# Optimization experiments

Measured on AMD Instinct MI355X. Metric: run time of the kernel, lower is better.

Reference implementation:

```python
import jax, jax.numpy as jnp
import numpy as np

D_MODEL = 1024
H = 16
D_K = D_MODEL // H
D_FF = 4096
EPS = 1e-5
NEG = -1e9


def setup_inputs() -> dict:
    key = jax.random.key(0)
    ks = jax.random.split(key, 12)
    B, S = 4, 1024
    s = 1.0 / np.sqrt(D_MODEL)
    inp = {
        'x': jax.random.normal(ks[0], (B, S, D_MODEL), dtype=jnp.float32),
        'src_mask': jax.random.randint(ks[1], (B, 1, 1, S), 0, 2, dtype=jnp.int32),
        'wq': jax.random.normal(ks[2], (D_MODEL, D_MODEL), dtype=jnp.float32) * s,
        'bq': jnp.zeros((D_MODEL,), jnp.float32),
        'wk': jax.random.normal(ks[3], (D_MODEL, D_MODEL), dtype=jnp.float32) * s,
        'bk': jnp.zeros((D_MODEL,), jnp.float32),
        'wv': jax.random.normal(ks[4], (D_MODEL, D_MODEL), dtype=jnp.float32) * s,
        'bv': jnp.zeros((D_MODEL,), jnp.float32),
        'wo': jax.random.normal(ks[5], (D_MODEL, D_MODEL), dtype=jnp.float32) * s,
        'bo': jnp.zeros((D_MODEL,), jnp.float32),
        'w1': jax.random.normal(ks[6], (D_MODEL, D_FF), dtype=jnp.float32) * s,
        'b1': jnp.zeros((D_FF,), jnp.float32),
        'w2': jax.random.normal(ks[7], (D_FF, D_MODEL), dtype=jnp.float32) * (1.0 / np.sqrt(D_FF)),
        'b2': jnp.zeros((D_MODEL,), jnp.float32),
        'ln1_a': jnp.ones((1,), jnp.float32),
        'ln1_b': jnp.zeros((1,), jnp.float32),
        'ln2_a': jnp.ones((1,), jnp.float32),
        'ln2_b': jnp.zeros((1,), jnp.float32),
    }
    return inp


def _layernorm(x, alpha, bias):
    # Matches torch: mean over last dim; std is UNBIASED (ddof=1); divide by (std + eps).
    mean = jnp.mean(x, axis=-1, keepdims=True)
    std = jnp.sqrt(jnp.var(x, axis=-1, keepdims=True, ddof=1))
    return alpha * (x - mean) / (std + EPS) + bias


def _attention(xn, src_mask, wq, bq, wk, bk, wv, bv, wo, bo):
    B, S, _ = xn.shape
    q = (xn @ wq + bq).reshape(B, S, H, D_K).transpose(0, 2, 1, 3)  # [B,H,S,Dk]
    k = (xn @ wk + bk).reshape(B, S, H, D_K).transpose(0, 2, 1, 3)
    v = (xn @ wv + bv).reshape(B, S, H, D_K).transpose(0, 2, 1, 3)
    scores = jnp.einsum('bhqd,bhkd->bhqk', q, k) / np.sqrt(D_K)
    scores = jnp.where(src_mask == 0, NEG, scores)
    # NOTE: original module applies NO softmax (faithful to source).
    out = jnp.einsum('bhqk,bhkd->bhqd', scores, v)  # [B,H,S,Dk]
    out = out.transpose(0, 2, 1, 3).reshape(B, S, D_MODEL)
    return out @ wo + bo


def reference(x, src_mask, wq, bq, wk, bk, wv, bv, wo, bo,
              w1, b1, w2, b2, ln1_a, ln1_b, ln2_a, ln2_b):
    # Pre-norm residual 1: self-attention
    x = x + _attention(_layernorm(x, ln1_a, ln1_b), src_mask,
                       wq, bq, wk, bk, wv, bv, wo, bo)
    # Pre-norm residual 2: FFN
    xn = _layernorm(x, ln2_a, ln2_b)
    ffn = jax.nn.relu(xn @ w1 + b1) @ w2 + b2
    return x + ffn
```

## Files before the change

kernel.cpp:

```cpp
#include <hip/hip_runtime.h>
#include <hip/hip_bf16.h>
#include <math.h>


#define EPS 1e-5f

typedef __attribute__((ext_vector_type(8))) short bf16x8;
typedef __attribute__((ext_vector_type(4))) float f32x4;
typedef __attribute__((ext_vector_type(8))) int i32x8;
typedef __attribute__((ext_vector_type(4))) int i32x4;

typedef const __attribute__((address_space(1))) unsigned char glob_byte;
typedef __attribute__((address_space(3))) unsigned char lds_byte;

__device__ __forceinline__ void g2l16(const void* g, void* l) {
  __builtin_amdgcn_global_load_lds((glob_byte*)g, (lds_byte*)l, 16, 0, 0);
}

__device__ __forceinline__ unsigned short f2bf(float f) {
  union { float f; unsigned int u; } v; v.f = f;
  return (unsigned short)((v.u + 0x7FFFu + ((v.u >> 16) & 1u)) >> 16);
}
__device__ __forceinline__ float bf2f(unsigned short b) {
  union { unsigned int u; float f; } v; v.u = (unsigned int)b << 16;
  return v.f;
}
__device__ __forceinline__ unsigned int pk_fp8x4(float a, float b, float c, float d) {
  unsigned int p = 0;
  p = __builtin_amdgcn_cvt_pk_fp8_f32(a, b, p, false);
  p = __builtin_amdgcn_cvt_pk_fp8_f32(c, d, p, true);
  return p;
}
__device__ __forceinline__ unsigned char f2f8(float v) {
  return (unsigned char)(__builtin_amdgcn_cvt_pk_fp8_f32(v, v, 0, false) & 0xFF);
}
__device__ __forceinline__ unsigned fp4enc(float v) {
  const float a = fabsf(v);
  unsigned c = (unsigned)(a >= 0.25f) + (unsigned)(a >= 0.75f) +
               (unsigned)(a >= 1.25f) + (unsigned)(a >= 1.75f) +
               (unsigned)(a >= 2.5f) + (unsigned)(a >= 3.5f) +
               (unsigned)(a >= 5.0f);
  return c | (v < 0.f ? 8u : 0u);
}

__global__ __launch_bounds__(256) void wconv_ln_kernel(
    const float* __restrict__ wq, const float* __restrict__ wk,
    const float* __restrict__ wv, const float* __restrict__ wo,
    const float* __restrict__ w1, const float* __restrict__ w2,
    const float* __restrict__ bq, const float* __restrict__ bk,
    const float* __restrict__ bv, const float* __restrict__ bo,
    unsigned char* __restrict__ wqkvF4, unsigned short* __restrict__ woT,
    unsigned short* __restrict__ wvT16,
    unsigned char* __restrict__ w1F4, unsigned char* __restrict__ w2F4,
    float* __restrict__ bqkv, float* __restrict__ cboW,
    const float* __restrict__ x, unsigned char* __restrict__ xnF4,
    unsigned short* __restrict__ xn16,
    const float* __restrict__ ln1a, const float* __restrict__ ln1b) {
  __shared__ float tile[64][65];
  const int bid = blockIdx.x;
  const int t = threadIdx.x;
  if (bid >= 3073) {
    const int row = bid - 3073;
    const float4 v = ((const float4*)(x + (size_t)row * 1024))[t];
    float s  = v.x + v.y + v.z + v.w;
    float ss = v.x * v.x + v.y * v.y + v.z * v.z + v.w * v.w;
#pragma unroll
    for (int off = 32; off > 0; off >>= 1) {
      s  += __shfl_down(s, off, 64);
      ss += __shfl_down(ss, off, 64);
    }
    __shared__ float red[8];
    const int lane = t & 63, wv_ = t >> 6;
    if (lane == 0) { red[wv_] = s; red[4 + wv_] = ss; }
    __syncthreads();
    const float S  = red[0] + red[1] + red[2] + red[3];
    const float SS = red[4] + red[5] + red[6] + red[7];
    const float mean = S * (1.0f / 1024.0f);
    float var = (SS - 1024.0f * mean * mean) * (1.0f / 1023.0f);
    var = fmaxf(var, 0.0f);
    const float scl = ln1a[0] / (sqrtf(var) + EPS);
    const float b = ln1b[0];
    const float o0 = (v.x - mean) * scl + b;
    const float o1 = (v.y - mean) * scl + b;
    const float o2 = (v.z - mean) * scl + b;
    const float o3 = (v.w - mean) * scl + b;
    ((unsigned short*)xnF4)[(size_t)row * 256 + t] = (unsigned short)(
        fp4enc(o0) | (fp4enc(o1) << 4) | (fp4enc(o2) << 8) | (fp4enc(o3) << 12));
    ushort4 o4;
    o4.x = f2bf(o0); o4.y = f2bf(o1); o4.z = f2bf(o2); o4.w = f2bf(o3);
    ((ushort4*)(xn16 + (size_t)row * 1024))[t] = o4;
    return;
  }
  if (bid == 3072) {
#pragma unroll
    for (int i = 0; i < 12; ++i) {
      const int n = i * 256 + t;
      bqkv[n] = n < 1024 ? bq[n] : (n < 2048 ? bk[n - 1024] : bv[n - 2048]);
    }
#pragma unroll
    for (int i = 0; i < 16; ++i) {
      const int idx = i * 256 + t;
      cboW[idx] = bo[idx & 1023];
    }
    return;
  }
  const float* src; int K, N, tk, tn;
  float ps = 32.f;
  unsigned short* dst16 = nullptr; unsigned char* dst4 = nullptr;
  unsigned short* dstv = nullptr;
  if (bid < 1024) {
    const int m = bid >> 8, loc = bid & 255;
    src = m == 0 ? wq : m == 1 ? wk : m == 2 ? wv : wo;
    if (m == 3) dst16 = woT;
    else { dst4 = wqkvF4 + (size_t)m * 1024 * 512; if (m == 2) dstv = wvT16; }
    K = 1024; N = 1024; tk = loc >> 4; tn = loc & 15;
  } else if (bid < 2048) {
    const int loc = bid - 1024; src = w1; dst4 = w1F4;
    K = 1024; N = 4096; tk = loc >> 6; tn = loc & 63;
  } else {
    const int loc = bid - 2048; src = w2; dst4 = w2F4; ps = 64.f;
    K = 4096; N = 1024; tk = loc >> 4; tn = loc & 15;
  }
  const int lr = t >> 4, lc = (t & 15) * 4;
#pragma unroll
  for (int i = 0; i < 4; ++i) {
    const float4 v = *(const float4*)(src + (size_t)(tk * 64 + lr + 16 * i) * N + tn * 64 + lc);
    tile[lr + 16 * i][lc + 0] = v.x;
    tile[lr + 16 * i][lc + 1] = v.y;
    tile[lr + 16 * i][lc + 2] = v.z;
    tile[lr + 16 * i][lc + 3] = v.w;
  }
  __syncthreads();
  const int on = t >> 2, ok = (t & 3) * 16;
#pragma unroll
  for (int jj = 0; jj < 4; ++jj) {
    if (dst4) {
      const unsigned e0 = fp4enc(tile[ok + 4 * jj + 0][on] * ps);
      const unsigned e1 = fp4enc(tile[ok + 4 * jj + 1][on] * ps);
      const unsigned e2 = fp4enc(tile[ok + 4 * jj + 2][on] * ps);
      const unsigned e3 = fp4enc(tile[ok + 4 * jj + 3][on] * ps);
      *(unsigned short*)(dst4 + (size_t)(tn * 64 + on) * (K >> 1) +
                         ((tk * 64 + ok + 4 * jj) >> 1)) =
          (unsigned short)(e0 | (e1 << 4) | (e2 << 8) | (e3 << 12));
      if (dstv) {
        ushort4 o4;
        o4.x = f2bf(tile[ok + 4 * jj + 0][on]);
        o4.y = f2bf(tile[ok + 4 * jj + 1][on]);
        o4.z = f2bf(tile[ok + 4 * jj + 2][on]);
        o4.w = f2bf(tile[ok + 4 * jj + 3][on]);
        *(ushort4*)(dstv + (size_t)(tn * 64 + on) * 1024 + tk * 64 + ok + 4 * jj) = o4;
      }
    } else {
      ushort4 o4;
      o4.x = f2bf(tile[ok + 4 * jj + 0][on]);
      o4.y = f2bf(tile[ok + 4 * jj + 1][on]);
      o4.z = f2bf(tile[ok + 4 * jj + 2][on]);
      o4.w = f2bf(tile[ok + 4 * jj + 3][on]);
      *(ushort4*)(dst16 + (size_t)(tn * 64 + on) * K + tk * 64 + ok + 4 * jj) = o4;
    }
  }
}

__global__ __launch_bounds__(256) void msum_kernel(
    const unsigned short* __restrict__ xn16, const int* __restrict__ mask,
    float* __restrict__ partials, float* __restrict__ nmp) {
  const int blk = blockIdx.x, b = blk >> 4, rc = blk & 15;
  const int t = threadIdx.x;
  const int row0 = b * 1024 + rc * 64;
  float4 s = {0.f, 0.f, 0.f, 0.f};
  float cnt = 0.f;
#pragma unroll 4
  for (int r = 0; r < 64; ++r) {
    const int row = row0 + r;
    if (mask[row] == 0) {
      const ushort4 v = ((const ushort4*)(xn16 + (size_t)row * 1024))[t];
      s.x += bf2f(v.x); s.y += bf2f(v.y); s.z += bf2f(v.z); s.w += bf2f(v.w);
      cnt += 1.f;
    }
  }
  ((float4*)(partials + (size_t)blk * 1024))[t] = s;
  if (t == 0) nmp[blk] = cnt;
}

template <int EPI, int TN, int RX, int RY, unsigned SB>
__global__ __launch_bounds__(256, 4) void mfma_gemm_fp4(
    const unsigned char* __restrict__ A, const unsigned char* __restrict__ Bt,
    const float* __restrict__ bias, const void* __restrict__ resv,
    void* __restrict__ C0, void* __restrict__ C1, const int* __restrict__ maskG,
    int N, int ldab, int ldbb, int KB) {
  constexpr int NSPAN = TN / 2;
  constexpr int NJ = NSPAN / 16;
  __shared__ __align__(16) unsigned char As[128 * 128];
  __shared__ __align__(16) unsigned char Bs[TN * 128];
  const int tid = threadIdx.x, lane = tid & 63;
  const int w = tid >> 6;
  const int quad = lane >> 4, col = lane & 15;
  const int wm = w & 1, wn = w >> 1;

  int bx = blockIdx.x, by = blockIdx.y;
  {
    const int gx = gridDim.x;
    const int L = bx + gx * by;
    const int r = L & 7, s = L >> 3;
    const int nrx = gx / RX;
    const int rx = r % nrx, ry = r / nrx;
    bx = rx * RX + s % RX;
    by = ry * RY + (s / RX) % RY;
  }
  const int m0 = by * 128, n0 = bx * TN;

  f32x4 acc[4][NJ];
  const f32x4 z4 = {0.f, 0.f, 0.f, 0.f};
#pragma unroll
  for (int i = 0; i < 4; ++i)
#pragma unroll
    for (int j = 0; j < NJ; ++j) acc[i][j] = z4;

  for (int k0 = 0; k0 < KB; k0 += 128) {
    __syncthreads();
#pragma unroll
    for (int t = 0; t < 4; ++t) {
      const int s = t * 256 + tid;
      const int r = s >> 3, c = (s & 7) ^ (r & 7);
      g2l16(A + (size_t)(m0 + r) * ldab + k0 + c * 16, (void*)(As + s * 16));
    }
#pragma unroll
    for (int t = 0; t < TN / 32; ++t) {
      const int s = t * 256 + tid;
      const int r = s >> 3, c = (s & 7) ^ (r & 7);
      g2l16(Bt + (size_t)(n0 + r) * ldbb + k0 + c * 16, (void*)(Bs + s * 16));
    }
    __syncthreads();
#pragma unroll
    for (int kk = 0; kk < 2; ++kk) {
      i32x8 af[4];
#pragma unroll
      for (int i = 0; i < 4; ++i) {
        const int rr = wm * 64 + i * 16 + col;
        const i32x4* rowp = (const i32x4*)(As + rr * 128);
        const i32x4 q = rowp[(kk * 4 + quad) ^ (rr & 7)];
        af[i] = __builtin_shufflevector(q, q, 0, 1, 2, 3, 4, 5, 6, 7);
      }
#pragma unroll
      for (int j = 0; j < NJ; ++j) {
        const int rr = wn * NSPAN + j * 16 + col;
        const i32x4* rowp = (const i32x4*)(Bs + rr * 128);
        const i32x4 q = rowp[(kk * 4 + quad) ^ (rr & 7)];
        const i32x8 bfj = __builtin_shufflevector(q, q, 0, 1, 2, 3, 4, 5, 6, 7);
#pragma unroll
        for (int i = 0; i < 4; ++i)
          acc[i][j] = __builtin_amdgcn_mfma_scale_f32_16x16x128_f8f6f4(
              af[i], bfj, acc[i][j], 4, 4, 0, 0x7F7F7F7Fu, 0, SB);
      }
    }
  }
#pragma unroll
  for (int i = 0; i < 4; ++i) {
    const int mrow = m0 + wm * 64 + i * 16 + quad * 4;
#pragma unroll
    for (int j = 0; j < NJ; ++j) {
      const int n = n0 + wn * NSPAN + j * 16 + col;
      const float bn = bias[n];
      if (EPI == 2) {
        if (n0 >= 1024) {
          float v0 = acc[i][j][0] + bn;
          float v1 = acc[i][j][1] + bn;
          float v2 = acc[i][j][2] + bn;
          float v3 = acc[i][j][3] + bn;
          if (n0 < 2048) {
            const int4 mq = *(const int4*)(maskG + mrow);
            v0 = mq.x ? v0 : 0.f;
            v1 = mq.y ? v1 : 0.f;
            v2 = mq.z ? v2 : 0.f;
            v3 = mq.w ? v3 : 0.f;
          }
          *(unsigned int*)((unsigned char*)C1 + (size_t)(n - 1024) * 4096 + mrow) =
              pk_fp8x4(v0, v1, v2, v3);
        } else {
#pragma unroll
          for (int r = 0; r < 4; ++r)
            ((unsigned char*)C0)[(size_t)(mrow + r) * N + n] = f2f8(acc[i][j][r] + bn);
        }
        continue;
      }
#pragma unroll
      for (int r = 0; r < 4; ++r) {
        const int m = mrow + r;
        if (EPI == 0) {
          const float v = fmaxf(acc[i][j][r] + bn, 0.f);
          const unsigned e = fp4enc(v);
          const unsigned eo = __shfl_down(e, 1, 64);
          if (!(lane & 1))
            ((unsigned char*)C0)[(size_t)m * (N >> 1) + (n >> 1)] =
                (unsigned char)(e | (eo << 4));
        } else {
          const float v = acc[i][j][r] + bn + bf2f(((const unsigned short*)resv)[(size_t)m * N + n]);
          ((float*)C0)[(size_t)m * N + n] = v;
        }
      }
    }
  }
}

template <int EPI, int TN, int RX, int RY>
__global__ __launch_bounds__(256, 4) void mfma_gemm_fp8(
    const unsigned char* __restrict__ A, const unsigned char* __restrict__ Bt,
    const float* __restrict__ bias, const void* __restrict__ resv,
    void* __restrict__ C0, void* __restrict__ C1, const int* __restrict__ maskG,
    int N, int lda, int ldb, int KH) {
  constexpr int NSPAN = TN / 2;
  constexpr int NJ = NSPAN / 16;
  __shared__ __align__(16) unsigned char As[128 * 128];
  __shared__ __align__(16) unsigned char Bs[TN * 128];
  const int tid = threadIdx.x, lane = tid & 63;
  const int w = tid >> 6;
  const int quad = lane >> 4, col = lane & 15;
  const int wm = w & 1, wn = w >> 1;

  int bx = blockIdx.x, by = blockIdx.y;
  {
    const int gx = gridDim.x;
    const int L = bx + gx * by;
    const int r = L & 7, s = L >> 3;
    const int nrx = gx / RX;
    const int rx = r % nrx, ry = r / nrx;
    bx = rx * RX + s % RX;
    by = ry * RY + (s / RX) % RY;
  }
  const int m0 = by * 128, n0 = bx * TN;
  const unsigned char* Bt2 = Bt;
  const float* bias2 = bias;
  if (EPI == 3) {
    const int bb = m0 >> 10;
    Bt2 += (size_t)bb * 1024 * ldb;
    bias2 += bb * 1024;
  }

  f32x4 acc[4][NJ];
  const f32x4 z4 = {0.f, 0.f, 0.f, 0.f};
#pragma unroll
  for (int i = 0; i < 4; ++i)
#pragma unroll
    for (int j = 0; j < NJ; ++j) acc[i][j] = z4;

  for (int k0 = 0; k0 < KH; k0 += 128) {
    __syncthreads();
#pragma unroll
    for (int t = 0; t < 4; ++t) {
      const int s = t * 256 + tid;
      const int r = s >> 3, c = (s & 7) ^ (r & 7);
      g2l16(A + (size_t)(m0 + r) * lda + k0 + c * 16, (void*)(As + s * 16));
    }
#pragma unroll
    for (int t = 0; t < TN / 32; ++t) {
      const int s = t * 256 + tid;
      const int r = s >> 3, c = (s & 7) ^ (r & 7);
      g2l16(Bt2 + (size_t)(n0 + r) * ldb + k0 + c * 16, (void*)(Bs + s * 16));
    }
    __syncthreads();
    i32x8 af[4];
#pragma unroll
    for (int i = 0; i < 4; ++i) {
      const int rr = wm * 64 + i * 16 + col;
      const i32x4* rowp = (const i32x4*)(As + rr * 128);
      const i32x4 lo = rowp[(2 * quad) ^ (rr & 7)];
      const i32x4 hi = rowp[(2 * quad + 1) ^ (rr & 7)];
      af[i] = __builtin_shufflevector(lo, hi, 0, 1, 2, 3, 4, 5, 6, 7);
    }
#pragma unroll
    for (int j = 0; j < NJ; ++j) {
      const int rr = wn * NSPAN + j * 16 + col;
      const i32x4* rowp = (const i32x4*)(Bs + rr * 128);
      const i32x4 lo = rowp[(2 * quad) ^ (rr & 7)];
      const i32x4 hi = rowp[(2 * quad + 1) ^ (rr & 7)];
      const i32x8 bfj = __builtin_shufflevector(lo, hi, 0, 1, 2, 3, 4, 5, 6, 7);
#pragma unroll
      for (int i = 0; i < 4; ++i)
        acc[i][j] = __builtin_amdgcn_mfma_scale_f32_16x16x128_f8f6f4(
            af[i], bfj, acc[i][j], 0, 0, 0, 0x7F7F7F7Fu, 0, 0x7F7F7F7Fu);
    }
  }
#pragma unroll
  for (int i = 0; i < 4; ++i) {
    const int mrow = m0 + wm * 64 + i * 16 + quad * 4;
#pragma unroll
    for (int j = 0; j < NJ; ++j) {
      const int n = n0 + wn * NSPAN + j * 16 + col;
      const float bn = bias2[n];
#pragma unroll
      for (int r = 0; r < 4; ++r) {
        const int m = mrow + r;
        const float v = acc[i][j][r] + bn + ((const float*)resv)[(size_t)m * N + n];
        ((unsigned short*)C0)[(size_t)m * N + n] = f2bf(v);
      }
    }
  }
}

__global__ __launch_bounds__(256) void ln2_kernel(
    const unsigned short* __restrict__ x1,
    const float* __restrict__ alpha, const float* __restrict__ beta,
    unsigned char* __restrict__ xn2f4) {
  const int row = blockIdx.x, t = threadIdx.x;
  const size_t i = (size_t)row * 256 + t;
  const ushort4 a4 = ((const ushort4*)x1)[i];
  float4 v;
  v.x = bf2f(a4.x); v.y = bf2f(a4.y); v.z = bf2f(a4.z); v.w = bf2f(a4.w);
  float s  = v.x + v.y + v.z + v.w;
  float ss = v.x * v.x + v.y * v.y + v.z * v.z + v.w * v.w;
#pragma unroll
  for (int off = 32; off > 0; off >>= 1) {
    s  += __shfl_down(s, off, 64);
    ss += __shfl_down(ss, off, 64);
  }
  __shared__ float red[8];
  const int lane = t & 63, wv_ = t >> 6;
  if (lane == 0) { red[wv_] = s; red[4 + wv_] = ss; }
  __syncthreads();
  const float S  = red[0] + red[1] + red[2] + red[3];
  const float SS = red[4] + red[5] + red[6] + red[7];
  const float mean = S * (1.0f / 1024.0f);
  float var = (SS - 1024.0f * mean * mean) * (1.0f / 1023.0f);
  var = fmaxf(var, 0.0f);
  const float scl = alpha[0] / (sqrtf(var) + EPS);
  const float bb = beta[0];
  const float o0 = (v.x - mean) * scl + bb;
  const float o1 = (v.y - mean) * scl + bb;
  const float o2 = (v.z - mean) * scl + bb;
  const float o3 = (v.w - mean) * scl + bb;
  ((unsigned short*)xn2f4)[i] = (unsigned short)(
      fp4enc(o0) | (fp4enc(o1) << 4) | (fp4enc(o2) << 8) | (fp4enc(o3) << 12));
}

__global__ __launch_bounds__(512) void moment_kernel(
    const unsigned char* __restrict__ kvT8, const unsigned short* __restrict__ woT,
    const unsigned short* __restrict__ wvT16, const float* __restrict__ bqkv,
    const float* __restrict__ partials, const float* __restrict__ nmp,
    unsigned char* __restrict__ Wbt8, float* __restrict__ cboW) {
  __shared__ __align__(16) unsigned char Ks[64 * 512];
  __shared__ __align__(16) unsigned char Vs[64 * 512];
  __shared__ __align__(16) unsigned short Ms[64 * 64];
  __shared__ float sS[1024];
  __shared__ float corrS[64];
  const int tid = threadIdx.x, lane = tid & 63, w = tid >> 6;
  const int quad = lane >> 4, col = lane & 15;
  const int bh = blockIdx.x, b = bh >> 4, h = bh & 15;
  const int w4 = w & 3, ch = w >> 2;
  const f32x4 z4 = {0.f, 0.f, 0.f, 0.f};
  const size_t kb = (size_t)(h * 64) * 4096 + b * 1024;
  const size_t vb = (size_t)(1024 + h * 64) * 4096 + b * 1024;

#pragma unroll
  for (int i = 0; i < 4; ++i) {
    const int s = i * 512 + tid;
    const int r = s >> 5, c = (s & 31) ^ (r & 31);
    g2l16(kvT8 + kb + (size_t)r * 4096 + c * 16, (void*)(Ks + s * 16));
    g2l16(kvT8 + vb + (size_t)r * 4096 + c * 16, (void*)(Vs + s * 16));
  }
  {
    float2 sacc = {0.f, 0.f};
#pragma unroll
    for (int rc = 0; rc < 16; ++rc) {
      const float2 p = ((const float2*)(partials + (size_t)(b * 16 + rc) * 1024))[tid];
      sacc.x += p.x; sacc.y += p.y;
    }
    ((float2*)sS)[tid] = sacc;
  }
  float nm = 0.f;
#pragma unroll
  for (int i = 0; i < 16; ++i) nm += nmp[b * 16 + i];
  __syncthreads();

  {
    const int d2 = tid >> 3, kq = tid & 7;
    const unsigned short* wrow = wvT16 + (size_t)(h * 64 + d2) * 1024 + kq * 128;
    float s = 0.f;
#pragma unroll
    for (int jj = 0; jj < 16; ++jj) {
      const bf16x8 w8 = *(const bf16x8*)(wrow + jj * 8);
      const float* sp = sS + kq * 128 + jj * 8;
      s += bf2f((unsigned short)w8[0]) * sp[0] + bf2f((unsigned short)w8[1]) * sp[1] +
           bf2f((unsigned short)w8[2]) * sp[2] + bf2f((unsigned short)w8[3]) * sp[3] +
           bf2f((unsigned short)w8[4]) * sp[4] + bf2f((unsigned short)w8[5]) * sp[5] +
           bf2f((unsigned short)w8[6]) * sp[6] + bf2f((unsigned short)w8[7]) * sp[7];
    }
    s += __shfl_xor(s, 1, 64);
    s += __shfl_xor(s, 2, 64);
    s += __shfl_xor(s, 4, 64);
    if ((lane & 7) == 0) corrS[d2] = s + nm * bqkv[2048 + h * 64 + d2];
  }

  f32x4 acc[2] = {z4, z4};
  const int rr = w4 * 16 + col;
#pragma unroll 1
  for (int st = 0; st < 2; ++st) {
    if (st) {
      __syncthreads();
#pragma unroll
      for (int i = 0; i < 4; ++i) {
        const int s = i * 512 + tid;
        const int r = s >> 5, c = (s & 31) ^ (r & 31);
        g2l16(kvT8 + kb + (size_t)r * 4096 + 512 + c * 16, (void*)(Ks + s * 16));
        g2l16(kvT8 + vb + (size_t)r * 4096 + 512 + c * 16, (void*)(Vs + s * 16));
      }
      __syncthreads();
    }
#pragma unroll
    for (int q = 0; q < 4; ++q) {
      const i32x4* rowpK = (const i32x4*)(Ks + rr * 512);
      const i32x4 klo = rowpK[(q * 8 + 2 * quad) ^ (rr & 31)];
      const i32x4 khi = rowpK[(q * 8 + 2 * quad + 1) ^ (rr & 31)];
      const i32x8 af = __builtin_shufflevector(klo, khi, 0, 1, 2, 3, 4, 5, 6, 7);
#pragma unroll
      for (int cl = 0; cl < 2; ++cl) {
        const int vr = (ch * 2 + cl) * 16 + col;
        const i32x4* rowpV = (const i32x4*)(Vs + vr * 512);
        const i32x4 vlo = rowpV[(q * 8 + 2 * quad) ^ (vr & 31)];
        const i32x4 vhi = rowpV[(q * 8 + 2 * quad + 1) ^ (vr & 31)];
        const i32x8 vf = __builtin_shufflevector(vlo, vhi, 0, 1, 2, 3, 4, 5, 6, 7);
        acc[cl] = __builtin_amdgcn_mfma_scale_f32_16x16x128_f8f6f4(
            af, vf, acc[cl], 0, 0, 0, 0x7F7F7F7Fu, 0, 0x7F7F7F7Fu);
      }
    }
  }
#pragma unroll
  for (int cl = 0; cl < 2; ++cl) {
    const int d2 = (ch * 2 + cl) * 16 + col;
#pragma unroll
    for (int r = 0; r < 4; ++r) {
      const int d1 = w4 * 16 + quad * 4 + r;
      Ms[d1 * 64 + ((d2 >> 3) ^ (d1 & 7)) * 8 + (d2 & 7)] = f2bf(0.125f * acc[cl][r]);
    }
  }
  __syncthreads();

  unsigned char* Wb8 = Wbt8 + (size_t)b * 1048576;
#pragma unroll 1
  for (int nt8 = 0; nt8 < 8; ++nt8) {
    const int nbase = (w * 8 + nt8) * 16;
    const bf16x8 af0 = *(const bf16x8*)(woT + (size_t)(nbase + col) * 1024 + h * 64 + quad * 8);
    const bf16x8 af1 = *(const bf16x8*)(woT + (size_t)(nbase + col) * 1024 + h * 64 + 32 + quad * 8);
#pragma unroll
    for (int dt = 0; dt < 4; ++dt) {
      const int d1r = dt * 16 + col;
      const bf16x8 bf0 = *(const bf16x8*)(Ms + d1r * 64 + ((quad ^ (d1r & 7)) * 8));
      const bf16x8 bf1 = *(const bf16x8*)(Ms + d1r * 64 + (((4 + quad) ^ (d1r & 7)) * 8));
      f32x4 a = __builtin_amdgcn_mfma_f32_16x16x32_bf16(af0, bf0, z4, 0, 0, 0);
      a = __builtin_amdgcn_mfma_f32_16x16x32_bf16(af1, bf1, a, 0, 0, 0);
#pragma unroll
      for (int r = 0; r < 4; ++r)
        Wb8[(size_t)(nbase + quad * 4 + r) * 1024 + h * 64 + dt * 16 + col] = f2f8(a[r]);
    }
  }
#pragma unroll
  for (int rep = 0; rep < 2; ++rep) {
    const int n = rep * 512 + tid;
    const unsigned short* wrow = woT + (size_t)n * 1024 + h * 64;
    float s = 0.f;
#pragma unroll
    for (int k = 0; k < 64; k += 8) {
      const bf16x8 w8 = *(const bf16x8*)(wrow + k);
      s += bf2f((unsigned short)w8[0]) * corrS[k + 0] +
           bf2f((unsigned short)w8[1]) * corrS[k + 1] +
           bf2f((unsigned short)w8[2]) * corrS[k + 2] +
           bf2f((unsigned short)w8[3]) * corrS[k + 3] +
           bf2f((unsigned short)w8[4]) * corrS[k + 4] +
           bf2f((unsigned short)w8[5]) * corrS[k + 5] +
           bf2f((unsigned short)w8[6]) * corrS[k + 6] +
           bf2f((unsigned short)w8[7]) * corrS[k + 7];
    }
    atomicAdd(cboW + b * 1024 + n, -1e9f * s);
  }
}

extern "C" void kernel_launch(void* const* d_in, const int* in_sizes, int n_in,
                              void* d_out, int out_size, void* d_ws, size_t ws_size,
                              hipStream_t stream) {
  const float* x    = (const float*)d_in[0];
  const int*   mask = (const int*)d_in[1];
  const float* wq = (const float*)d_in[2];
  const float* bq = (const float*)d_in[3];
  const float* wk = (const float*)d_in[4];
  const float* bk = (const float*)d_in[5];
  const float* wv = (const float*)d_in[6];
  const float* bv = (const float*)d_in[7];
  const float* wo = (const float*)d_in[8];
  const float* bo = (const float*)d_in[9];
  const float* w1 = (const float*)d_in[10];
  const float* b1 = (const float*)d_in[11];
  const float* w2 = (const float*)d_in[12];
  const float* b2 = (const float*)d_in[13];
  const float* ln1a = (const float*)d_in[14];
  const float* ln1b = (const float*)d_in[15];
  const float* ln2a = (const float*)d_in[16];
  const float* ln2b = (const float*)d_in[17];
  float* out = (float*)d_out;
  char* W = (char*)d_ws;
  const size_t MB = 1u << 20;

  unsigned char*  wqkvF4 = (unsigned char*)(W + 0 * MB);
  unsigned short* woT    = (unsigned short*)(W + 2 * MB);
  unsigned short* wvT16  = (unsigned short*)(W + 4 * MB);
  unsigned char*  w1F4   = (unsigned char*)(W + 6 * MB);
  unsigned char*  w2F4   = (unsigned char*)(W + 8 * MB);
  float*          bqkv   = (float*)(W + 10 * MB);
  float*          cboW   = (float*)(W + 10 * MB + 65536);
  float*          partials = (float*)(W + 10 * MB + 131072);
  float*          nmp    = (float*)(W + 10 * MB + 458752);
  unsigned char*  xnF4   = (unsigned char*)(W + 11 * MB);
  unsigned char*  Q8     = (unsigned char*)(W + 13 * MB);
  unsigned char*  kvT8   = (unsigned char*)(W + 17 * MB);
  unsigned char*  Wbt8   = (unsigned char*)(W + 25 * MB);
  unsigned short* x1     = (unsigned short*)(W + 29 * MB);
  unsigned short* xn16   = (unsigned short*)(W + 37 * MB);
  unsigned char*  xn2f4  = (unsigned char*)(W + 45 * MB);
  unsigned char*  hbF4   = (unsigned char*)(W + 47 * MB);

  wconv_ln_kernel<<<7169, 256, 0, stream>>>(wq, wk, wv, wo, w1, w2, bq, bk, bv, bo,
                                            wqkvF4, woT, wvT16, w1F4, w2F4,
                                            bqkv, cboW, x, xnF4, xn16, ln1a, ln1b);
  msum_kernel<<<64, 256, 0, stream>>>(xn16, mask, partials, nmp);
  mfma_gemm_fp4<2, 128, 12, 8, 0x7A7A7A7AU><<<dim3(24, 32), 256, 0, stream>>>(
      xnF4, wqkvF4, bqkv, nullptr, Q8, kvT8, mask, 1024, 512, 512, 512);
  moment_kernel<<<64, 512, 0, stream>>>(kvT8, woT, wvT16, bqkv, partials, nmp,
                                        Wbt8, cboW);
  mfma_gemm_fp8<3, 64, 8, 8><<<dim3(16, 32), 256, 0, stream>>>(
      Q8, Wbt8, cboW, x, x1, nullptr, nullptr, 1024, 1024, 1024, 1024);
  ln2_kernel<<<4096, 256, 0, stream>>>(x1, ln2a, ln2b, xn2f4);
  mfma_gemm_fp4<0, 128, 16, 8, 0x7A7A7A7AU><<<dim3(32, 32), 256, 0, stream>>>(
      xn2f4, w1F4, b1, nullptr, hbF4, nullptr, nullptr, 4096, 512, 512, 512);
  mfma_gemm_fp4<1, 64, 8, 8, 0x79797979U><<<dim3(16, 32), 256, 0, stream>>>(
      hbF4, w2F4, b2, x1, out, nullptr, nullptr, 1024, 2048, 2048, 2048);
}
```

Before: 244.4 us.

## Double-buffer LDS in FP4/FP8 GEMMs and fold masked-sum into QKV GEMM launch

Both MFMA GEMM kernels now keep two LDS stages. The next K-tile is issued with global_load_lds while the current one is computed, using explicit vmcnt waits and raw barriers in place of two __syncthreads per iteration. The separate msum kernel is removed. Its work runs in 64 extra blocks appended to the QKV GEMM grid, which saves one launch. Launch-bound occupancy hints are lowered to 2 and 3 because LDS use doubles, so fewer blocks fit per CU.

```diff
diff --git a/kernel.cpp b/kernel.cpp
--- a/kernel.cpp
+++ b/kernel.cpp
@@ -161,41 +161,47 @@
   }
 }
 
-__global__ __launch_bounds__(256) void msum_kernel(
-    const unsigned short* __restrict__ xn16, const int* __restrict__ mask,
-    float* __restrict__ partials, float* __restrict__ nmp) {
-  const int blk = blockIdx.x, b = blk >> 4, rc = blk & 15;
-  const int t = threadIdx.x;
-  const int row0 = b * 1024 + rc * 64;
-  float4 s = {0.f, 0.f, 0.f, 0.f};
-  float cnt = 0.f;
-#pragma unroll 4
-  for (int r = 0; r < 64; ++r) {
-    const int row = row0 + r;
-    if (mask[row] == 0) {
-      const ushort4 v = ((const ushort4*)(xn16 + (size_t)row * 1024))[t];
-      s.x += bf2f(v.x); s.y += bf2f(v.y); s.z += bf2f(v.z); s.w += bf2f(v.w);
-      cnt += 1.f;
-    }
-  }
-  ((float4*)(partials + (size_t)blk * 1024))[t] = s;
-  if (t == 0) nmp[blk] = cnt;
-}
-
 template <int EPI, int TN, int RX, int RY, unsigned SB>
-__global__ __launch_bounds__(256, 4) void mfma_gemm_fp4(
+__global__ __launch_bounds__(256, 2) void mfma_gemm_fp4(
     const unsigned char* __restrict__ A, const unsigned char* __restrict__ Bt,
     const float* __restrict__ bias, const void* __restrict__ resv,
     void* __restrict__ C0, void* __restrict__ C1, const int* __restrict__ maskG,
-    int N, int ldab, int ldbb, int KB) {
+    const unsigned short* __restrict__ xn16s, float* __restrict__ partials,
+    float* __restrict__ nmp, int N, int ldab, int ldbb, int KB) {
   constexpr int NSPAN = TN / 2;
   constexpr int NJ = NSPAN / 16;
-  __shared__ __align__(16) unsigned char As[128 * 128];
-  __shared__ __align__(16) unsigned char Bs[TN * 128];
+  constexpr int ASZ = 128 * 128, BSZ = TN * 128;
+  __shared__ __align__(16) unsigned char As[2][ASZ];
+  __shared__ __align__(16) unsigned char Bs[2][BSZ];
   const int tid = threadIdx.x, lane = tid & 63;
   const int w = tid >> 6;
   const int quad = lane >> 4, col = lane & 15;
   const int wm = w & 1, wn = w >> 1;
+
+  if (EPI == 2) {
+    const int L0 = blockIdx.x + gridDim.x * blockIdx.y;
+    if (L0 >= 768) {
+      const int idx = L0 - 768;
+      if (idx < 64) {
+        const int b = idx >> 4, rc = idx & 15;
+        const int row0 = b * 1024 + rc * 64;
+        float4 s = {0.f, 0.f, 0.f, 0.f};
+        float cnt = 0.f;
+#pragma unroll 4
+        for (int r = 0; r < 64; ++r) {
+          const int row = row0 + r;
+          if (maskG[row] == 0) {
+            const ushort4 v = ((const ushort4*)(xn16s + (size_t)row * 1024))[tid];
+            s.x += bf2f(v.x); s.y += bf2f(v.y); s.z += bf2f(v.z); s.w += bf2f(v.w);
+            cnt += 1.f;
+          }
+        }
+        ((float4*)(partials + (size_t)idx * 1024))[tid] = s;
+        if (tid == 0) nmp[idx] = cnt;
+      }
+      return;
+    }
+  }
 
   int bx = blockIdx.x, by = blockIdx.y;
   {
@@ -216,35 +222,54 @@
 #pragma unroll
     for (int j = 0; j < NJ; ++j) acc[i][j] = z4;
 
-  for (int k0 = 0; k0 < KB; k0 += 128) {
-    __syncthreads();
+  auto STAGE = [&](int kt, int bufsel) {
+    const int k0 = kt * 128;
+    unsigned char* Ab = As[bufsel];
+    unsigned char* Bb = Bs[bufsel];
 #pragma unroll
     for (int t = 0; t < 4; ++t) {
       const int s = t * 256 + tid;
       const int r = s >> 3, c = (s & 7) ^ (r & 7);
-      g2l16(A + (size_t)(m0 + r) * ldab + k0 + c * 16, (void*)(As + s * 16));
+      g2l16(A + (size_t)(m0 + r) * ldab + k0 + c * 16, (void*)(Ab + s * 16));
     }
 #pragma unroll
     for (int t = 0; t < TN / 32; ++t) {
       const int s = t * 256 + tid;
       const int r = s >> 3, c = (s & 7) ^ (r & 7);
-      g2l16(Bt + (size_t)(n0 + r) * ldbb + k0 + c * 16, (void*)(Bs + s * 16));
-    }
-    __syncthreads();
+      g2l16(Bt + (size_t)(n0 + r) * ldbb + k0 + c * 16, (void*)(Bb + s * 16));
+    }
+  };
+
+  const int NT = KB >> 7;
+  STAGE(0, 0);
+  for (int kt = 0; kt < NT; ++kt) {
+    const int cur = kt & 1;
+    if (kt + 1 < NT) {
+      STAGE(kt + 1, cur ^ 1);
+      if constexpr (TN == 128)
+        asm volatile("s_waitcnt vmcnt(8)" ::: "memory");
+      else
+        asm volatile("s_waitcnt vmcnt(6)" ::: "memory");
+    } else {
+      asm volatile("s_waitcnt vmcnt(0)" ::: "memory");
+    }
+    __builtin_amdgcn_s_barrier();
+    const unsigned char* Ac = As[cur];
+    const unsigned char* Bc = Bs[cur];
 #pragma unroll
     for (int kk = 0; kk < 2; ++kk) {
       i32x8 af[4];
 #pragma unroll
       for (int i = 0; i < 4; ++i) {
         const int rr = wm * 64 + i * 16 + col;
-        const i32x4* rowp = (const i32x4*)(As + rr * 128);
+        const i32x4* rowp = (const i32x4*)(Ac + rr * 128);
         const i32x4 q = rowp[(kk * 4 + quad) ^ (rr & 7)];
         af[i] = __builtin_shufflevector(q, q, 0, 1, 2, 3, 4, 5, 6, 7);
       }
 #pragma unroll
       for (int j = 0; j < NJ; ++j) {
         const int rr = wn * NSPAN + j * 16 + col;
-        const i32x4* rowp = (const i32x4*)(Bs + rr * 128);
+        const i32x4* rowp = (const i32x4*)(Bc + rr * 128);
         const i32x4 q = rowp[(kk * 4 + quad) ^ (rr & 7)];
         const i32x8 bfj = __builtin_shufflevector(q, q, 0, 1, 2, 3, 4, 5, 6, 7);
 #pragma unroll
@@ -253,6 +278,8 @@
               af[i], bfj, acc[i][j], 4, 4, 0, 0x7F7F7F7Fu, 0, SB);
       }
     }
+    asm volatile("" ::: "memory");
+    __builtin_amdgcn_s_barrier();
   }
 #pragma unroll
   for (int i = 0; i < 4; ++i) {
@@ -303,15 +330,16 @@
 }
 
 template <int EPI, int TN, int RX, int RY>
-__global__ __launch_bounds__(256, 4) void mfma_gemm_fp8(
+__global__ __launch_bounds__(256, 3) void mfma_gemm_fp8(
     const unsigned char* __restrict__ A, const unsigned char* __restrict__ Bt,
     const float* __restrict__ bias, const void* __restrict__ resv,
     void* __restrict__ C0, void* __restrict__ C1, const int* __restrict__ maskG,
     int N, int lda, int ldb, int KH) {
   constexpr int NSPAN = TN / 2;
   constexpr int NJ = NSPAN / 16;
-  __shared__ __align__(16) unsigned char As[128 * 128];
-  __shared__ __align__(16) unsigned char Bs[TN * 128];
+  constexpr int ASZ = 128 * 128, BSZ = TN * 128;
+  __shared__ __align__(16) unsigned char As[2][ASZ];
+  __shared__ __align__(16) unsigned char Bs[2][BSZ];
   const int tid = threadIdx.x, lane = tid & 63;
   const int w = tid >> 6;
   const int quad = lane >> 4, col = lane & 15;
@@ -343,26 +371,42 @@
 #pragma unroll
     for (int j = 0; j < NJ; ++j) acc[i][j] = z4;
 
-  for (int k0 = 0; k0 < KH; k0 += 128) {
-    __syncthreads();
+  auto STAGE = [&](int kt, int bufsel) {
+    const int k0 = kt * 128;
+    unsigned char* Ab = As[bufsel];
+    unsigned char* Bb = Bs[bufsel];
 #pragma unroll
     for (int t = 0; t < 4; ++t) {
       const int s = t * 256 + tid;
       const int r = s >> 3, c = (s & 7) ^ (r & 7);
-      g2l16(A + (size_t)(m0 + r) * lda + k0 + c * 16, (void*)(As + s * 16));
+      g2l16(A + (size_t)(m0 + r) * lda + k0 + c * 16, (void*)(Ab + s * 16));
     }
 #pragma unroll
     for (int t = 0; t < TN / 32; ++t) {
       const int s = t * 256 + tid;
       const int r = s >> 3, c = (s & 7) ^ (r & 7);
-      g2l16(Bt2 + (size_t)(n0 + r) * ldb + k0 + c * 16, (void*)(Bs + s * 16));
-    }
-    __syncthreads();
+      g2l16(Bt2 + (size_t)(n0 + r) * ldb + k0 + c * 16, (void*)(Bb + s * 16));
+    }
+  };
+
+  const int NT = KH >> 7;
+  STAGE(0, 0);
+  for (int kt = 0; kt < NT; ++kt) {
+    const int cur = kt & 1;
+    if (kt + 1 < NT) {
+      STAGE(kt + 1, cur ^ 1);
+      asm volatile("s_waitcnt vmcnt(6)" ::: "memory");
+    } else {
+      asm volatile("s_waitcnt vmcnt(0)" ::: "memory");
+    }
+    __builtin_amdgcn_s_barrier();
+    const unsigned char* Ac = As[cur];
+    const unsigned char* Bc = Bs[cur];
     i32x8 af[4];
 #pragma unroll
     for (int i = 0; i < 4; ++i) {
       const int rr = wm * 64 + i * 16 + col;
-      const i32x4* rowp = (const i32x4*)(As + rr * 128);
+      const i32x4* rowp = (const i32x4*)(Ac + rr * 128);
       const i32x4 lo = rowp[(2 * quad) ^ (rr & 7)];
       const i32x4 hi = rowp[(2 * quad + 1) ^ (rr & 7)];
       af[i] = __builtin_shufflevector(lo, hi, 0, 1, 2, 3, 4, 5, 6, 7);
@@ -370,7 +414,7 @@
 #pragma unroll
     for (int j = 0; j < NJ; ++j) {
       const int rr = wn * NSPAN + j * 16 + col;
-      const i32x4* rowp = (const i32x4*)(Bs + rr * 128);
+      const i32x4* rowp = (const i32x4*)(Bc + rr * 128);
       const i32x4 lo = rowp[(2 * quad) ^ (rr & 7)];
       const i32x4 hi = rowp[(2 * quad + 1) ^ (rr & 7)];
       const i32x8 bfj = __builtin_shufflevector(lo, hi, 0, 1, 2, 3, 4, 5, 6, 7);
@@ -379,6 +423,8 @@
         acc[i][j] = __builtin_amdgcn_mfma_scale_f32_16x16x128_f8f6f4(
             af[i], bfj, acc[i][j], 0, 0, 0, 0x7F7F7F7Fu, 0, 0x7F7F7F7Fu);
     }
+    asm volatile("" ::: "memory");
+    __builtin_amdgcn_s_barrier();
   }
 #pragma unroll
   for (int i = 0; i < 4; ++i) {
@@ -619,16 +665,18 @@
   wconv_ln_kernel<<<7169, 256, 0, stream>>>(wq, wk, wv, wo, w1, w2, bq, bk, bv, bo,
                                             wqkvF4, woT, wvT16, w1F4, w2F4,
                                             bqkv, cboW, x, xnF4, xn16, ln1a, ln1b);
-  msum_kernel<<<64, 256, 0, stream>>>(xn16, mask, partials, nmp);
-  mfma_gemm_fp4<2, 128, 12, 8, 0x7A7A7A7AU><<<dim3(24, 32), 256, 0, stream>>>(
-      xnF4, wqkvF4, bqkv, nullptr, Q8, kvT8, mask, 1024, 512, 512, 512);
+  mfma_gemm_fp4<2, 128, 12, 8, 0x7A7A7A7AU><<<dim3(24, 35), 256, 0, stream>>>(
+      xnF4, wqkvF4, bqkv, nullptr, Q8, kvT8, mask, xn16, partials, nmp,
+      1024, 512, 512, 512);
   moment_kernel<<<64, 512, 0, stream>>>(kvT8, woT, wvT16, bqkv, partials, nmp,
                                         Wbt8, cboW);
   mfma_gemm_fp8<3, 64, 8, 8><<<dim3(16, 32), 256, 0, stream>>>(
       Q8, Wbt8, cboW, x, x1, nullptr, nullptr, 1024, 1024, 1024, 1024);
   ln2_kernel<<<4096, 256, 0, stream>>>(x1, ln2a, ln2b, xn2f4);
   mfma_gemm_fp4<0, 128, 16, 8, 0x7A7A7A7AU><<<dim3(32, 32), 256, 0, stream>>>(
-      xn2f4, w1F4, b1, nullptr, hbF4, nullptr, nullptr, 4096, 512, 512, 512);
+      xn2f4, w1F4, b1, nullptr, hbF4, nullptr, nullptr, nullptr, nullptr, nullptr,
+      4096, 512, 512, 512);
   mfma_gemm_fp4<1, 64, 8, 8, 0x79797979U><<<dim3(16, 32), 256, 0, stream>>>(
-      hbF4, w2F4, b2, x1, out, nullptr, nullptr, 1024, 2048, 2048, 2048);
-}
+      hbF4, w2F4, b2, x1, out, nullptr, nullptr, nullptr, nullptr, nullptr,
+      1024, 2048, 2048, 2048);
+}
```

After: 243.9 us. About the same (-0.2%).
